# Kernel optimization log

Measured on AMD Instinct MI355X. Metric: run time of the kernel, lower is better.

Reference implementation:

```python
import jax, jax.numpy as jnp
import numpy as np

B, N, D_IN, D_HID, D_OUT = 64, 512, 512, 512, 512


def setup_inputs() -> dict:
    key = jax.random.key(0)
    ks = jax.random.split(key, 8)
    gain = 0.02  # xavier_normal_ gain used in reset_parameters_xavier

    def xavier(k, fan_in, fan_out):
        std = gain * np.sqrt(2.0 / (fan_in + fan_out))
        return jax.random.normal(k, (fan_in, fan_out), dtype=jnp.float32) * std

    return {
        "batch_graph": jax.random.normal(ks[0], (B, N, D_IN), dtype=jnp.float32),
        "adj": jax.random.uniform(ks[1], (B, N, N), dtype=jnp.float32),
        "W1": xavier(ks[2], D_IN, D_HID),
        "b1": jnp.zeros((D_HID,), dtype=jnp.float32),
        "W2": xavier(ks[3], D_HID, D_HID),
        "b2": jnp.zeros((D_HID,), dtype=jnp.float32),
        "W3": xavier(ks[4], D_HID, D_OUT),
        "b3": jnp.zeros((D_OUT,), dtype=jnp.float32),
    }


def _normalize_adj(adj):
    # rowsum^-0.5 with inf -> 0 (original: torch.pow then isinf mask)
    rowsum = adj.sum(axis=1)                       # [B, N] (sum over dim 1, as in torch)
    safe = jnp.where(rowsum == 0, 1.0, rowsum)
    r = jnp.where(rowsum == 0, 0.0, safe ** -0.5)  # [B, N]
    # (adj @ D)^T @ D = D @ adj^T @ D with D = diag(r)
    return r[:, :, None] * jnp.swapaxes(adj, 1, 2) * r[:, None, :]


def reference(batch_graph, adj, W1, b1, W2, b2, W3, b3):
    # Block-diagonal big_adj @ big_graph == per-graph batched matmul.
    A = _normalize_adj(adj)  # [B, N, N]

    def gc(x, W, b):
        # support = x @ W ; output = A @ support + b
        return jnp.einsum('bij,bjd->bid', A, x @ W) + b

    # dropout is identity in eval mode (deterministic reference)
    x = jax.nn.relu(gc(batch_graph, W1, b1))
    x = jax.nn.relu(gc(x, W2, b2))
    return gc(x, W3, b3)  # [B, N, D_OUT]
```

## Files before the change

kernel.cpp:

```cpp
#include <hip/hip_runtime.h>
#include <cstdint>
#include <cstddef>

typedef _Float16 f16;
typedef _Float16 f16x4 __attribute__((ext_vector_type(4)));
typedef _Float16 f16x8 __attribute__((ext_vector_type(8)));
typedef float    f32x4 __attribute__((ext_vector_type(4)));

#define NB 64
#define NN 262144

__device__ __forceinline__ void gload_lds16(const void* g, void* l) {
    __builtin_amdgcn_global_load_lds(
        (const __attribute__((address_space(1))) void*)g,
        (__attribute__((address_space(3))) void*)l, 16, 0, 0);
}

__global__ __launch_bounds__(256)
void k_prep(const float* __restrict__ adj, f16* __restrict__ A_raw,
            float* __restrict__ part,
            const float* __restrict__ W1, const float* __restrict__ W2,
            const float* __restrict__ W3, f16* __restrict__ Wt,
            const float* __restrict__ X0, f16* __restrict__ Xa) {
    __shared__ float t[64][68];
    __shared__ float red[4][64];
    const int bid = blockIdx.x, tid = threadIdx.x;
    if (bid < 4096) {
        const int xcd = bid & 7, loc = bid >> 3;
        const int b = xcd * 8 + (loc >> 6);
        const int tile = loc & 63;
        const int i0 = (tile >> 3) * 64, j0 = (tile & 7) * 64;
        const int jt = tile & 7;
        const float* ab = adj + (size_t)b * NN;
        int trow = tid >> 4;
        int tc4  = (tid & 15) * 4;
        #pragma unroll
        for (int s = 0; s < 4; ++s) {
            int rr = trow + s * 16;
            *(f32x4*)&t[rr][tc4] = *(const f32x4*)&ab[(size_t)(j0 + rr) * 512 + i0 + tc4];
        }
        __syncthreads();
        {
            int c = tid & 63, g = tid >> 6;
            float sg = 0.f;
            #pragma unroll
            for (int s = 0; s < 16; ++s) sg += t[g * 16 + s][c];
            red[g][c] = sg;
        }
        f16* Ab = A_raw + (size_t)b * NN;
        int jq = (tid & 15) * 4;
        int ib = tid >> 4;
        #pragma unroll
        for (int s = 0; s < 4; ++s) {
            int ii = ib + s * 16;
            f16x4 o;
            #pragma unroll
            for (int q = 0; q < 4; ++q) o[q] = (f16)t[jq + q][ii];
            *(f16x4*)&Ab[(size_t)(i0 + ii) * 512 + j0 + jq] = o;
        }
        __syncthreads();
        if (tid < 64)
            part[((size_t)b * 8 + jt) * 512 + i0 + tid] =
                red[0][tid] + red[1][tid] + red[2][tid] + red[3][tid];
    } else if (bid < 4288) {
        int cb = bid - 4096;
        int z = cb >> 6, rem = cb & 63;
        const float* W = z == 0 ? W1 : (z == 1 ? W2 : W3);
        f16* out = Wt + (size_t)z * NN;
        int k0 = (rem >> 3) * 64, d0 = (rem & 7) * 64;
        int c = tid & 63, r4 = tid >> 6;
        #pragma unroll
        for (int s = 0; s < 16; ++s) {
            int rr = r4 + s * 4;
            t[rr][c] = W[(size_t)(k0 + rr) * 512 + d0 + c];
        }
        __syncthreads();
        int kq = (tid & 15) * 4;
        int db = tid >> 4;
        #pragma unroll
        for (int s = 0; s < 4; ++s) {
            int dd = db + s * 16;
            f16x4 o;
            #pragma unroll
            for (int q = 0; q < 4; ++q)
                o[q] = (f16)(64.f * t[kq + q][dd]);
            *(f16x4*)&out[(size_t)(d0 + dd) * 512 + k0 + kq] = o;
        }
    } else {
        size_t i = ((size_t)(bid - 4288) * 256 + tid) * 8;
        float4 v0 = *(const float4*)(X0 + i);
        float4 v1 = *(const float4*)(X0 + i + 4);
        f16x8 o;
        o[0] = (f16)v0.x; o[1] = (f16)v0.y; o[2] = (f16)v0.z; o[3] = (f16)v0.w;
        o[4] = (f16)v1.x; o[5] = (f16)v1.y; o[6] = (f16)v1.z; o[7] = (f16)v1.w;
        *(f16x8*)(Xa + i) = o;
    }
}

template<bool BIAS, bool RELU, bool OUTF32, bool RM, bool RN>
__global__ __launch_bounds__(256, 2)
void gemm_tn_ct(const f16* __restrict__ P, size_t pstr,
                const f16* __restrict__ Qt, size_t qstr,
                void* __restrict__ Cout, size_t cstr,
                const float* __restrict__ bias, const float* __restrict__ part,
                float iscale, float oscale) {
    __shared__ __align__(16) f16 Plds[2][8192];
    __shared__ __align__(16) f16 Qlds[2][8192];
    __shared__ float rs_lds[128];

    const int tid  = threadIdx.x;
    const int lane = tid & 63;
    const int wid  = tid >> 6;
    const int wm   = wid >> 1;
    const int wn   = wid & 1;

    const int wg  = blockIdx.x;
    const int swz = (wg & 7) * 128 + (wg >> 3);
    const int b   = swz >> 4;
    const int tt  = swz & 15;
    const int m0  = (tt >> 2) * 128;
    const int n0  = (tt & 3) * 128;

    const f16* Pb = P + (size_t)b * pstr;
    const f16* Qb = Qt + (size_t)b * qstr;

    const int srow = tid >> 3;
    const int sswz = (tid & 7) ^ (srow & 7);

    const int fr  = lane & 15;
    const int fs  = lane >> 4;
    const int fx  = fr & 7;

    auto stage = [&](const f16* __restrict__ Gb, int row0, f16* lds, int k0) {
        #pragma unroll
        for (int r = 0; r < 4; ++r) {
            const f16* src = Gb + (size_t)(row0 + r * 32 + srow) * 512 + k0 + sswz * 8;
            gload_lds16(src, lds + r * 2048 + tid * 8);
        }
    };

    f32x4 acc[4][4] = {};

    stage(Pb, m0, &Plds[0][0], 0);
    stage(Qb, n0, &Qlds[0][0], 0);

    if ((RM || RN) && tid < 128) {
        const float* p = part + (size_t)b * 4096 + (RM ? m0 : n0) + tid;
        float s = 0.f;
        #pragma unroll
        for (int jt = 0; jt < 8; ++jt) s += p[jt * 512];
        rs_lds[tid] = (s > 0.f) ? rsqrtf(s) : 0.f;
    }

    for (int t = 0; t < 8; ++t) {
        const int nb = t & 1;
        if (t < 7) {
            stage(Pb, m0, &Plds[nb ^ 1][0], (t + 1) * 64);
            stage(Qb, n0, &Qlds[nb ^ 1][0], (t + 1) * 64);
            asm volatile("s_waitcnt vmcnt(8)" ::: "memory");
        } else {
            asm volatile("s_waitcnt vmcnt(0)" ::: "memory");
        }
        __builtin_amdgcn_s_barrier();

        const f16* Pl = &Plds[nb][0];
        const f16* Ql = &Qlds[nb][0];
        #pragma unroll
        for (int krep = 0; krep < 2; ++krep) {
            const int sp = ((fs + krep * 4) ^ fx) * 8;
            f16x8 af[4], bf[4];
            #pragma unroll
            for (int mi = 0; mi < 4; ++mi)
                af[mi] = *(const f16x8*)&Pl[(wm * 64 + mi * 16 + fr) * 64 + sp];
            #pragma unroll
            for (int ni = 0; ni < 4; ++ni)
                bf[ni] = *(const f16x8*)&Ql[(wn * 64 + ni * 16 + fr) * 64 + sp];
            __builtin_amdgcn_s_setprio(1);
            #pragma unroll
            for (int mi = 0; mi < 4; ++mi)
                #pragma unroll
                for (int ni = 0; ni < 4; ++ni)
                    acc[mi][ni] = __builtin_amdgcn_mfma_f32_16x16x32_f16(
                        af[mi], bf[ni], acc[mi][ni], 0, 0, 0);
            __builtin_amdgcn_s_setprio(0);
        }
        asm volatile("s_waitcnt lgkmcnt(0)" ::: "memory");
        __builtin_amdgcn_sched_barrier(0);
        __builtin_amdgcn_s_barrier();
    }

    const int cmb = (lane >> 4) * 4;
    f32x4 rm4[4];
    float rn1[4];
    if (RM) {
        #pragma unroll
        for (int mi = 0; mi < 4; ++mi)
            rm4[mi] = *(const f32x4*)&rs_lds[wm * 64 + mi * 16 + cmb];
    }
    if (RN) {
        #pragma unroll
        for (int ni = 0; ni < 4; ++ni)
            rn1[ni] = rs_lds[wn * 64 + ni * 16 + fr];
    }
    #pragma unroll
    for (int mi = 0; mi < 4; ++mi) {
        #pragma unroll
        for (int ni = 0; ni < 4; ++ni) {
            const int n = n0 + wn * 64 + ni * 16 + fr;
            const int m = m0 + wm * 64 + mi * 16 + cmb;
            float v[4];
            #pragma unroll
            for (int q = 0; q < 4; ++q) {
                float x = acc[mi][ni][q] * iscale;
                if (RM) x *= rm4[mi][q];
                if (RN) x *= rn1[ni];
                if (BIAS) x += bias[m + q];
                if (RELU) x = fmaxf(x, 0.f);
                v[q] = x * oscale;
            }
            if (OUTF32) {
                float* Cb = (float*)Cout + (size_t)b * cstr;
                f32x4 o; o[0] = v[0]; o[1] = v[1]; o[2] = v[2]; o[3] = v[3];
                *(f32x4*)&Cb[(size_t)n * 512 + m] = o;
            } else {
                f16* Cb = (f16*)Cout + (size_t)b * cstr;
                f16x4 o; o[0] = (f16)v[0]; o[1] = (f16)v[1]; o[2] = (f16)v[2]; o[3] = (f16)v[3];
                *(f16x4*)&Cb[(size_t)n * 512 + m] = o;
            }
        }
    }
}

extern "C" void kernel_launch(void* const* d_in, const int* in_sizes, int n_in,
                              void* d_out, int out_size, void* d_ws, size_t ws_size,
                              hipStream_t stream) {
    const float* X0  = (const float*)d_in[0];
    const float* adj = (const float*)d_in[1];
    const float* W1  = (const float*)d_in[2];
    const float* b1  = (const float*)d_in[3];
    const float* W2  = (const float*)d_in[4];
    const float* b2  = (const float*)d_in[5];
    const float* W3  = (const float*)d_in[6];
    const float* b3  = (const float*)d_in[7];

    uint8_t* ws = (uint8_t*)d_ws;
    float* part = (float*)ws;
    f16* Wt1 = (f16*)(ws + (1 << 20));
    f16* A_raw = (f16*)(ws + (1 << 20) + (size_t)3 * NN * 2);
    f16* Xa  = A_raw + (size_t)NB * NN;
    f16* S_t = Xa + (size_t)NB * NN;

    k_prep<<<dim3(12480), dim3(256), 0, stream>>>(adj, A_raw, part, W1, W2, W3, Wt1, X0, Xa);

    dim3 gg(1024), gb(256);
    gemm_tn_ct<false, false, false, true,  false><<<gg, gb, 0, stream>>>(Xa,  (size_t)NN, Wt1, (size_t)0,  S_t, (size_t)NN, nullptr, part, 4.f, 1.f);
    gemm_tn_ct<true,  true,  false, false, true ><<<gg, gb, 0, stream>>>(S_t, (size_t)NN, A_raw, (size_t)NN, Xa, (size_t)NN, b1, part, 1.f / 256.f, 256.f);
    gemm_tn_ct<false, false, false, true,  false><<<gg, gb, 0, stream>>>(Xa,  (size_t)NN, Wt1 + NN, (size_t)0,  S_t, (size_t)NN, nullptr, part, 16.f, 1.f);
    gemm_tn_ct<true,  true,  false, false, true ><<<gg, gb, 0, stream>>>(S_t, (size_t)NN, A_raw, (size_t)NN, Xa, (size_t)NN, b2, part, 1.f / 262144.f, 256.f);
    gemm_tn_ct<false, false, false, true,  false><<<gg, gb, 0, stream>>>(Xa,  (size_t)NN, Wt1 + 2 * NN, (size_t)0,  S_t, (size_t)NN, nullptr, part, 16.f, 1.f);
    gemm_tn_ct<true,  false, true,  false, true ><<<gg, gb, 0, stream>>>(S_t, (size_t)NN, A_raw, (size_t)NN, d_out, (size_t)NN, b3, part, 1.f / 262144.f, 1.f);
}
```

Before: 215.4 us.

## Fuse per-layer support and aggregation GEMMs into one kernel with 512-thread blocks

```diff
diff --git a/kernel.cpp b/kernel.cpp
--- a/kernel.cpp
+++ b/kernel.cpp
@@ -14,6 +14,10 @@
     __builtin_amdgcn_global_load_lds(
         (const __attribute__((address_space(1))) void*)g,
         (__attribute__((address_space(3))) void*)l, 16, 0, 0);
+}
+
+__device__ __forceinline__ int SWC(int row, int col) {
+    return ((((col >> 2) ^ (row >> 2)) & 15) << 2) | (col & 3);
 }
 
 __global__ __launch_bounds__(256)
@@ -22,7 +26,7 @@
             const float* __restrict__ W1, const float* __restrict__ W2,
             const float* __restrict__ W3, f16* __restrict__ Wt,
             const float* __restrict__ X0, f16* __restrict__ Xa) {
-    __shared__ float t[64][68];
+    __shared__ float t[4096];
     __shared__ float red[4][64];
     const int bid = blockIdx.x, tid = threadIdx.x;
     if (bid < 4096) {
@@ -37,14 +41,18 @@
         #pragma unroll
         for (int s = 0; s < 4; ++s) {
             int rr = trow + s * 16;
-            *(f32x4*)&t[rr][tc4] = *(const f32x4*)&ab[(size_t)(j0 + rr) * 512 + i0 + tc4];
+            *(f32x4*)&t[rr * 64 + SWC(rr, tc4)] =
+                *(const f32x4*)&ab[(size_t)(j0 + rr) * 512 + i0 + tc4];
         }
         __syncthreads();
         {
             int c = tid & 63, g = tid >> 6;
             float sg = 0.f;
             #pragma unroll
-            for (int s = 0; s < 16; ++s) sg += t[g * 16 + s][c];
+            for (int s = 0; s < 16; ++s) {
+                int row = g * 16 + s;
+                sg += t[row * 64 + SWC(row, c)];
+            }
             red[g][c] = sg;
         }
         f16* Ab = A_raw + (size_t)b * NN;
@@ -55,7 +63,8 @@
             int ii = ib + s * 16;
             f16x4 o;
             #pragma unroll
-            for (int q = 0; q < 4; ++q) o[q] = (f16)t[jq + q][ii];
+            for (int q = 0; q < 4; ++q)
+                o[q] = (f16)t[(jq + q) * 64 + SWC(jq + q, ii)];
             *(f16x4*)&Ab[(size_t)(i0 + ii) * 512 + j0 + jq] = o;
         }
         __syncthreads();
@@ -72,7 +81,7 @@
         #pragma unroll
         for (int s = 0; s < 16; ++s) {
             int rr = r4 + s * 4;
-            t[rr][c] = W[(size_t)(k0 + rr) * 512 + d0 + c];
+            t[rr * 64 + SWC(rr, c)] = W[(size_t)(k0 + rr) * 512 + d0 + c];
         }
         __syncthreads();
         int kq = (tid & 15) * 4;
@@ -83,7 +92,7 @@
             f16x4 o;
             #pragma unroll
             for (int q = 0; q < 4; ++q)
-                o[q] = (f16)(64.f * t[kq + q][dd]);
+                o[q] = (f16)(64.f * t[(kq + q) * 64 + SWC(kq + q, dd)]);
             *(f16x4*)&out[(size_t)(d0 + dd) * 512 + k0 + kq] = o;
         }
     } else {
@@ -98,54 +107,33 @@
 }
 
 template<bool BIAS, bool RELU, bool OUTF32, bool RM, bool RN>
-__global__ __launch_bounds__(256, 2)
-void gemm_tn_ct(const f16* __restrict__ P, size_t pstr,
-                const f16* __restrict__ Qt, size_t qstr,
-                void* __restrict__ Cout, size_t cstr,
-                const float* __restrict__ bias, const float* __restrict__ part,
-                float iscale, float oscale) {
-    __shared__ __align__(16) f16 Plds[2][8192];
-    __shared__ __align__(16) f16 Qlds[2][8192];
-    __shared__ float rs_lds[128];
-
+__device__ __forceinline__ void gemm_body(
+    f16* PL, f16* QL, float* rs_lds,
+    const f16* __restrict__ Pb, const f16* __restrict__ Qb, void* __restrict__ Cb,
+    const float* __restrict__ bias, const float* __restrict__ partb,
+    float iscale, float oscale, int m0, int n0) {
     const int tid  = threadIdx.x;
     const int lane = tid & 63;
     const int wid  = tid >> 6;
-    const int wm   = wid >> 1;
-    const int wn   = wid & 1;
-
-    const int wg  = blockIdx.x;
-    const int swz = (wg & 7) * 128 + (wg >> 3);
-    const int b   = swz >> 4;
-    const int tt  = swz & 15;
-    const int m0  = (tt >> 2) * 128;
-    const int n0  = (tt & 3) * 128;
-
-    const f16* Pb = P + (size_t)b * pstr;
-    const f16* Qb = Qt + (size_t)b * qstr;
-
-    const int srow = tid >> 3;
-    const int sswz = (tid & 7) ^ (srow & 7);
-
-    const int fr  = lane & 15;
-    const int fs  = lane >> 4;
-    const int fx  = fr & 7;
+    const int wm   = wid >> 2;
+    const int wn   = wid & 3;
+    const int fr = lane & 15, fs = lane >> 4, fx = fr & 7;
 
     auto stage = [&](const f16* __restrict__ Gb, int row0, f16* lds, int k0) {
         #pragma unroll
-        for (int r = 0; r < 4; ++r) {
-            const f16* src = Gb + (size_t)(row0 + r * 32 + srow) * 512 + k0 + sswz * 8;
-            gload_lds16(src, lds + r * 2048 + tid * 8);
+        for (int r = 0; r < 2; ++r) {
+            const f16* src = Gb + (size_t)(row0 + r * 64 + (tid >> 3)) * 512 + k0
+                           + (((tid & 7) ^ ((tid >> 3) & 7)) * 8);
+            gload_lds16(src, lds + r * 4096 + tid * 8);
         }
     };
 
-    f32x4 acc[4][4] = {};
-
-    stage(Pb, m0, &Plds[0][0], 0);
-    stage(Qb, n0, &Qlds[0][0], 0);
+    f32x4 acc[4][2] = {};
+    stage(Pb, m0, PL, 0);
+    stage(Qb, n0, QL, 0);
 
     if ((RM || RN) && tid < 128) {
-        const float* p = part + (size_t)b * 4096 + (RM ? m0 : n0) + tid;
+        const float* p = partb + (RM ? m0 : n0) + tid;
         float s = 0.f;
         #pragma unroll
         for (int jt = 0; jt < 8; ++jt) s += p[jt * 512];
@@ -155,31 +143,31 @@
     for (int t = 0; t < 8; ++t) {
         const int nb = t & 1;
         if (t < 7) {
-            stage(Pb, m0, &Plds[nb ^ 1][0], (t + 1) * 64);
-            stage(Qb, n0, &Qlds[nb ^ 1][0], (t + 1) * 64);
-            asm volatile("s_waitcnt vmcnt(8)" ::: "memory");
+            stage(Pb, m0, PL + (nb ^ 1) * 8192, (t + 1) * 64);
+            stage(Qb, n0, QL + (nb ^ 1) * 8192, (t + 1) * 64);
+            asm volatile("s_waitcnt vmcnt(4)" ::: "memory");
         } else {
             asm volatile("s_waitcnt vmcnt(0)" ::: "memory");
         }
         __builtin_amdgcn_s_barrier();
 
-        const f16* Pl = &Plds[nb][0];
-        const f16* Ql = &Qlds[nb][0];
+        const f16* Pl = PL + nb * 8192;
+        const f16* Ql = QL + nb * 8192;
         #pragma unroll
         for (int krep = 0; krep < 2; ++krep) {
             const int sp = ((fs + krep * 4) ^ fx) * 8;
-            f16x8 af[4], bf[4];
+            f16x8 af[4], bf[2];
             #pragma unroll
             for (int mi = 0; mi < 4; ++mi)
                 af[mi] = *(const f16x8*)&Pl[(wm * 64 + mi * 16 + fr) * 64 + sp];
             #pragma unroll
-            for (int ni = 0; ni < 4; ++ni)
-                bf[ni] = *(const f16x8*)&Ql[(wn * 64 + ni * 16 + fr) * 64 + sp];
+            for (int ni = 0; ni < 2; ++ni)
+                bf[ni] = *(const f16x8*)&Ql[(wn * 32 + ni * 16 + fr) * 64 + sp];
             __builtin_amdgcn_s_setprio(1);
             #pragma unroll
             for (int mi = 0; mi < 4; ++mi)
                 #pragma unroll
-                for (int ni = 0; ni < 4; ++ni)
+                for (int ni = 0; ni < 2; ++ni)
                     acc[mi][ni] = __builtin_amdgcn_mfma_f32_16x16x32_f16(
                         af[mi], bf[ni], acc[mi][ni], 0, 0, 0);
             __builtin_amdgcn_s_setprio(0);
@@ -191,7 +179,7 @@
 
     const int cmb = (lane >> 4) * 4;
     f32x4 rm4[4];
-    float rn1[4];
+    float rn1[2];
     if (RM) {
         #pragma unroll
         for (int mi = 0; mi < 4; ++mi)
@@ -199,14 +187,14 @@
     }
     if (RN) {
         #pragma unroll
-        for (int ni = 0; ni < 4; ++ni)
-            rn1[ni] = rs_lds[wn * 64 + ni * 16 + fr];
+        for (int ni = 0; ni < 2; ++ni)
+            rn1[ni] = rs_lds[wn * 32 + ni * 16 + fr];
     }
     #pragma unroll
     for (int mi = 0; mi < 4; ++mi) {
         #pragma unroll
-        for (int ni = 0; ni < 4; ++ni) {
-            const int n = n0 + wn * 64 + ni * 16 + fr;
+        for (int ni = 0; ni < 2; ++ni) {
+            const int n = n0 + wn * 32 + ni * 16 + fr;
             const int m = m0 + wm * 64 + mi * 16 + cmb;
             float v[4];
             #pragma unroll
@@ -219,15 +207,59 @@
                 v[q] = x * oscale;
             }
             if (OUTF32) {
-                float* Cb = (float*)Cout + (size_t)b * cstr;
                 f32x4 o; o[0] = v[0]; o[1] = v[1]; o[2] = v[2]; o[3] = v[3];
-                *(f32x4*)&Cb[(size_t)n * 512 + m] = o;
+                *(f32x4*)&((float*)Cb)[(size_t)n * 512 + m] = o;
             } else {
-                f16* Cb = (f16*)Cout + (size_t)b * cstr;
                 f16x4 o; o[0] = (f16)v[0]; o[1] = (f16)v[1]; o[2] = (f16)v[2]; o[3] = (f16)v[3];
-                *(f16x4*)&Cb[(size_t)n * 512 + m] = o;
+                *(f16x4*)&((f16*)Cb)[(size_t)n * 512 + m] = o;
             }
         }
+    }
+    __builtin_amdgcn_s_barrier();
+}
+
+template<int L>
+__global__ __launch_bounds__(512, 1)
+void k_layer(const f16* __restrict__ Xin, f16* __restrict__ S_t,
+             void* __restrict__ Xout, const f16* __restrict__ A_raw,
+             const f16* __restrict__ Wtz, const float* __restrict__ part,
+             const float* __restrict__ bias) {
+    __shared__ __align__(16) f16 Plds[2][8192];
+    __shared__ __align__(16) f16 Qlds[2][8192];
+    __shared__ float rs_lds[128];
+    const int wg  = blockIdx.x;
+    const int swz = (wg & 7) * 32 + (wg >> 3);
+    const int b   = swz >> 2;
+    const int d0  = (swz & 3) * 128;
+
+    const f16* Xb = Xin + (size_t)b * NN;
+    f16* Sb = S_t + (size_t)b * NN;
+    const f16* Ab = A_raw + (size_t)b * NN;
+    const float* pb = part + (size_t)b * 4096;
+
+    constexpr float is1 = (L == 0) ? 4.f : 16.f;
+    constexpr float is2 = (L == 0) ? (1.f / 256.f) : (1.f / 262144.f);
+    constexpr float os2 = (L == 2) ? 1.f : 256.f;
+
+    #pragma unroll 1
+    for (int mi = 0; mi < 4; ++mi)
+        gemm_body<false, false, false, true, false>(
+            &Plds[0][0], &Qlds[0][0], rs_lds, Xb, Wtz, Sb,
+            nullptr, pb, is1, 1.f, mi * 128, d0);
+
+    asm volatile("s_waitcnt vmcnt(0)" ::: "memory");
+    __builtin_amdgcn_s_barrier();
+
+    #pragma unroll 1
+    for (int ni = 0; ni < 4; ++ni) {
+        if (L == 2)
+            gemm_body<true, false, true, false, true>(
+                &Plds[0][0], &Qlds[0][0], rs_lds, Sb, Ab,
+                (float*)Xout + (size_t)b * NN, bias, pb, is2, os2, d0, ni * 128);
+        else
+            gemm_body<true, true, false, false, true>(
+                &Plds[0][0], &Qlds[0][0], rs_lds, Sb, Ab,
+                (f16*)Xout + (size_t)b * NN, bias, pb, is2, os2, d0, ni * 128);
     }
 }
 
@@ -249,14 +281,12 @@
     f16* A_raw = (f16*)(ws + (1 << 20) + (size_t)3 * NN * 2);
     f16* Xa  = A_raw + (size_t)NB * NN;
     f16* S_t = Xa + (size_t)NB * NN;
+    f16* Xd  = (f16*)d_out;
 
     k_prep<<<dim3(12480), dim3(256), 0, stream>>>(adj, A_raw, part, W1, W2, W3, Wt1, X0, Xa);
 
-    dim3 gg(1024), gb(256);
-    gemm_tn_ct<false, false, false, true,  false><<<gg, gb, 0, stream>>>(Xa,  (size_t)NN, Wt1, (size_t)0,  S_t, (size_t)NN, nullptr, part, 4.f, 1.f);
-    gemm_tn_ct<true,  true,  false, false, true ><<<gg, gb, 0, stream>>>(S_t, (size_t)NN, A_raw, (size_t)NN, Xa, (size_t)NN, b1, part, 1.f / 256.f, 256.f);
-    gemm_tn_ct<false, false, false, true,  false><<<gg, gb, 0, stream>>>(Xa,  (size_t)NN, Wt1 + NN, (size_t)0,  S_t, (size_t)NN, nullptr, part, 16.f, 1.f);
-    gemm_tn_ct<true,  true,  false, false, true ><<<gg, gb, 0, stream>>>(S_t, (size_t)NN, A_raw, (size_t)NN, Xa, (size_t)NN, b2, part, 1.f / 262144.f, 256.f);
-    gemm_tn_ct<false, false, false, true,  false><<<gg, gb, 0, stream>>>(Xa,  (size_t)NN, Wt1 + 2 * NN, (size_t)0,  S_t, (size_t)NN, nullptr, part, 16.f, 1.f);
-    gemm_tn_ct<true,  false, true,  false, true ><<<gg, gb, 0, stream>>>(S_t, (size_t)NN, A_raw, (size_t)NN, d_out, (size_t)NN, b3, part, 1.f / 262144.f, 1.f);
-}
+    dim3 gg(256), gb(512);
+    k_layer<0><<<gg, gb, 0, stream>>>(Xa, S_t, Xd,    A_raw, Wt1,          part, b1);
+    k_layer<1><<<gg, gb, 0, stream>>>(Xd, S_t, Xa,    A_raw, Wt1 + NN,     part, b2);
+    k_layer<2><<<gg, gb, 0, stream>>>(Xa, S_t, d_out, A_raw, Wt1 + 2 * NN, part, b3);
+}
```

New measurement: 248.9 us. 15.5% more time.
